# Optimization experiments

Hardware: AMD Instinct MI355X
Metric: run time of the kernel (lower is better)

## Reference

```python
import jax, jax.numpy as jnp
import numpy as np

B_, T_, D_ = 4, 4096, 512
H_, DH_ = 8, 64
N_HASHES, BUCKET = 4, 64
SELF_ATTN_VAL = -5e4  # TOKEN_SELF_ATTN_VALUE from reformer-pytorch


def setup_inputs() -> dict:
    key = jax.random.key(0)
    ks = jax.random.split(key, 12)
    s = 0.02
    return {
        "src": jax.random.normal(ks[0], (B_, T_, D_), jnp.float32),
        "Wqk": jax.random.normal(ks[1], (D_, D_), jnp.float32) * s,
        "Wv": jax.random.normal(ks[2], (D_, D_), jnp.float32) * s,
        "Wout": jax.random.normal(ks[3], (D_, D_), jnp.float32) * s,
        "bout": jnp.zeros((D_,), jnp.float32),
        "W1": jax.random.normal(ks[4], (D_, 2048), jnp.float32) * s,
        "b1": jnp.zeros((2048,), jnp.float32),
        "W2": jax.random.normal(ks[5], (2048, D_), jnp.float32) * s,
        "b2": jnp.zeros((D_,), jnp.float32),
        "gamma": jnp.ones((D_,), jnp.float32),
        "beta": jnp.zeros((D_,), jnp.float32),
        "rotations": jax.random.normal(ks[6], (DH_, N_HASHES, (T_ // BUCKET) // 2), jnp.float32),
    }


def _look_one_back(x):
    # concat each chunk with the previous chunk (wraparound), along the slot axis
    prev = jnp.concatenate([x[:, -1:], x[:, :-1]], axis=1)
    return jnp.concatenate([x, prev], axis=2)


def lsh_attention(qk, v, rotations):
    # qk, v: (B, T, d) with B = batch*heads; shared-QK LSH attention (non-causal,
    # attend_across_buckets=True, allow_duplicate_attention=True, no dropout)
    B, T, d = qk.shape
    n_buckets = T // BUCKET
    # --- hashing ---
    rv = jnp.einsum("btf,fhi->bhti", qk, rotations)          # (B, n_hashes, T, nb/2)
    rv = jnp.concatenate([rv, -rv], axis=-1)                  # (B, n_hashes, T, nb)
    buckets = jnp.argmax(rv, axis=-1)                         # (B, n_hashes, T)
    offsets = (jnp.arange(N_HASHES) * n_buckets)[None, :, None]
    buckets = (buckets + offsets).reshape(B, N_HASHES * T)
    # --- sort by (bucket, position) ---
    ticker = jnp.arange(N_HASHES * T)
    buckets_and_t = buckets * T + (ticker % T)[None, :]
    sticker = jnp.argsort(buckets_and_t, axis=-1)             # (B, n_hashes*T)
    undo_sort = jnp.argsort(sticker, axis=-1)
    st = sticker % T
    sqk = jnp.take_along_axis(qk, st[..., None], axis=1)      # (B, n_hashes*T, d)
    sv = jnp.take_along_axis(v, st[..., None], axis=1)
    # --- chunk ---
    chunks = N_HASHES * n_buckets
    bq_t = st.reshape(B, chunks, BUCKET)
    bqk = sqk.reshape(B, chunks, BUCKET, d)
    bv = sv.reshape(B, chunks, BUCKET, d)
    bq = bqk
    bk = bqk / (jnp.linalg.norm(bqk, axis=-1, keepdims=True) + 1e-6)
    bk = _look_one_back(bk)                                   # (B, chunks, 2*BUCKET, d)
    bv = _look_one_back(bv)
    bkv_t = _look_one_back(bq_t)                              # (B, chunks, 2*BUCKET)
    # --- attention within chunk (+ one look-back chunk) ---
    dots = jnp.einsum("bcie,bcje->bcij", bq, bk) * (d ** -0.5)
    self_mask = bq_t[:, :, :, None] == bkv_t[:, :, None, :]
    dots = jnp.where(self_mask, SELF_ATTN_VAL, dots)
    lse = jax.nn.logsumexp(dots, axis=-1, keepdims=True)
    p = jnp.exp(dots - lse)
    bo = jnp.einsum("bcij,bcje->bcie", p, bv)
    # --- unsort and combine hash rounds ---
    so = bo.reshape(B, N_HASHES * T, d)
    slog = lse.reshape(B, N_HASHES * T)
    o = jnp.take_along_axis(so, undo_sort[..., None], axis=1)
    logits = jnp.take_along_axis(slog, undo_sort, axis=1)
    o = o.reshape(B, N_HASHES, T, d)
    logits = logits.reshape(B, N_HASHES, T, 1)
    probs = jnp.exp(logits - jax.nn.logsumexp(logits, axis=1, keepdims=True))
    return jnp.sum(o * probs, axis=1)                         # (B, T, d)


def _layer(src, Wqk, Wv, Wout, bout, W1, b1, W2, b2, gamma, beta, rotations):
    b, t, dm = src.shape
    qk = src @ Wqk
    v = src @ Wv
    def split(x):
        return x.reshape(b, t, H_, DH_).transpose(0, 2, 1, 3).reshape(b * H_, t, DH_)
    o = lsh_attention(split(qk), split(v), rotations)
    o = o.reshape(b, H_, t, DH_).transpose(0, 2, 1, 3).reshape(b, t, dm)
    attn_out = o @ Wout + bout
    x = src + attn_out                # residual (dropout = identity in eval)
    ffn = jax.nn.relu(x @ W1 + b1) @ W2 + b2
    y = x + ffn
    mu = jnp.mean(y, axis=-1, keepdims=True)
    var = jnp.mean((y - mu) ** 2, axis=-1, keepdims=True)
    return (y - mu) / jnp.sqrt(var + 1e-6) * gamma + beta     # post-norm (norm2)


def reference(src, Wqk, Wv, Wout, bout, W1, b1, W2, b2, gamma, beta, rotations):
    return _layer(src, Wqk, Wv, Wout, bout, W1, b1, W2, b2, gamma, beta, rotations)
```

## Files before the change

kernel.cpp:

```cpp
#include <hip/hip_runtime.h>

#define B_ 4
#define T_ 4096
#define D_ 512
#define H_ 8
#define DH_ 64
#define NH_ 4
#define NB_ 64
#define BH_ (B_*H_)
#define CHUNKS_ (NH_*NB_)
#define NTICK_ (NH_*T_)
#define M_ (B_*T_)
#define FFN_ 2048

typedef __attribute__((ext_vector_type(8))) short bf16x8;
typedef __attribute__((ext_vector_type(4))) float f32x4;

__device__ __forceinline__ unsigned short f2bf(float x) {
  unsigned int u = __float_as_uint(x);
  return (unsigned short)((u + 0x7FFFu + ((u >> 16) & 1u)) >> 16);
}
__device__ __forceinline__ float bf2f(unsigned short s) {
  return __uint_as_float(((unsigned int)s) << 16);
}
__device__ __forceinline__ unsigned int cvt_pk_bf16(float lo, float hi) {
  unsigned int r;
  asm("v_cvt_pk_bf16_f32 %0, %1, %2" : "=v"(r) : "v"(lo), "v"(hi));
  return r;
}

__device__ __forceinline__ void gld_lds16(const void* g, void* l) {
  __builtin_amdgcn_global_load_lds(
      (const __attribute__((address_space(1))) unsigned int*)g,
      (__attribute__((address_space(3))) unsigned int*)l, 16, 0, 0);
}

__device__ __forceinline__ int off64(int row, int k) {
  return row * 64 + (((k >> 3) ^ ((row ^ (row >> 3)) & 7)) << 3) + (k & 7);
}
__device__ __forceinline__ int off128(int row, int k) {
  return row * 128 + (((k >> 3) ^ ((row ^ (row >> 3)) & 7)) << 3) + (k & 7);
}

template<int BM, int OUT_MODE, bool HAS_BIAS, bool RELU, bool HAS_RESID, bool FUSE_INV>
__global__ __launch_bounds__(256) void gemm_bf16(
    const unsigned short* __restrict__ A, const unsigned short* __restrict__ BT,
    const float* __restrict__ bias, const unsigned short* __restrict__ resid,
    float* __restrict__ Cf, unsigned short* __restrict__ Cb,
    float* __restrict__ invn,
    int M, int N, int K, int lda, int ldbt, int ldr)
{
  constexpr int MI = BM / 32;
  __shared__ __align__(16) unsigned short smem[(BM + 128) * 64];
  unsigned short* As = smem;
  unsigned short* Bs = smem + BM * 64;
  const int tid = threadIdx.x;
  const int lane = tid & 63;
  const int w = tid >> 6;
  const int wm = (w >> 1) * (BM / 2), wn = (w & 1) * 64;
  const int g = lane >> 4, cl = lane & 15;

  const int gx = gridDim.x;
  const int id = blockIdx.x + blockIdx.y * gx;
  const int cpx = (gx * gridDim.y) >> 3;
  const int swz = (id & 7) * cpx + (id >> 3);
  const int m0 = (swz / gx) * BM, n0 = (swz % gx) * 128;

  f32x4 acc[MI][4];
#pragma unroll
  for (int i = 0; i < MI; ++i)
#pragma unroll
    for (int j = 0; j < 4; ++j) acc[i][j] = (f32x4){0.f, 0.f, 0.f, 0.f};

  const int srow = tid >> 3;
  const int skc  = (tid & 7) * 8;

  for (int k0 = 0; k0 < K; k0 += 64) {
#pragma unroll
    for (int ci = 0; ci < BM / 32; ++ci)
      gld_lds16(&A[(size_t)(m0 + ci * 32 + srow) * lda + k0 + skc],
                &As[ci * 2048 + tid * 8]);
#pragma unroll
    for (int ci = 0; ci < 4; ++ci)
      gld_lds16(&BT[(size_t)(n0 + ci * 32 + srow) * ldbt + k0 + skc],
                &Bs[ci * 2048 + tid * 8]);
    __syncthreads();
#pragma unroll
    for (int kk = 0; kk < 64; kk += 32) {
      bf16x8 af[MI], bfr[4];
#pragma unroll
      for (int i = 0; i < MI; ++i)
        af[i] = *(const bf16x8*)&As[(wm + i * 16 + cl) * 64 + kk + g * 8];
#pragma unroll
      for (int j = 0; j < 4; ++j)
        bfr[j] = *(const bf16x8*)&Bs[(wn + j * 16 + cl) * 64 + kk + g * 8];
#pragma unroll
      for (int i = 0; i < MI; ++i)
#pragma unroll
        for (int j = 0; j < 4; ++j)
          acc[i][j] = __builtin_amdgcn_mfma_f32_16x16x32_bf16(af[i], bfr[j], acc[i][j], 0, 0, 0);
    }
    __syncthreads();
  }

  float bv[4];
  if constexpr (HAS_BIAS) {
#pragma unroll
    for (int j = 0; j < 4; ++j) bv[j] = bias[n0 + wn + j * 16 + cl];
  }
#pragma unroll
  for (int i = 0; i < MI; ++i) {
#pragma unroll
    for (int r = 0; r < 4; ++r) {
      const int lrow = wm + i * 16 + g * 4 + r;
      float v4[4];
      float ss = 0.f;
#pragma unroll
      for (int j = 0; j < 4; ++j) {
        float val = acc[i][j][r];
        if constexpr (HAS_BIAS) val += bv[j];
        if constexpr (RELU) val = fmaxf(val, 0.f);
        v4[j] = val;
        if constexpr (FUSE_INV) ss += val * val;
        if constexpr (OUT_MODE == 2)
          Cf[(size_t)(m0 + lrow) * N + n0 + wn + j * 16 + cl] = val;
      }
      const unsigned int p01 = cvt_pk_bf16(v4[0], v4[1]);
      const unsigned int p23 = cvt_pk_bf16(v4[2], v4[3]);
      const int sw = (lrow & 7) << 3;
      smem[lrow * 128 + ((wn +  0 + cl) ^ sw)] = (unsigned short)p01;
      smem[lrow * 128 + ((wn + 16 + cl) ^ sw)] = (unsigned short)(p01 >> 16);
      smem[lrow * 128 + ((wn + 32 + cl) ^ sw)] = (unsigned short)p23;
      smem[lrow * 128 + ((wn + 48 + cl) ^ sw)] = (unsigned short)(p23 >> 16);
      if constexpr (FUSE_INV) {
        ss += __shfl_xor(ss, 1); ss += __shfl_xor(ss, 2);
        ss += __shfl_xor(ss, 4); ss += __shfl_xor(ss, 8);
        if (cl == 0) {
          const int m = m0 + lrow;
          const int bb = m >> 12, t = m & (T_ - 1);
          const int hh = ((n0 + wn) >> 6) & 7;
          invn[((size_t)(bb * 8 + hh)) * T_ + t] = 1.0f / (sqrtf(ss) + 1e-6f);
        }
      }
    }
  }
  __syncthreads();
#pragma unroll
  for (int l = 0; l < BM / 16; ++l) {
    const int idx = tid + l * 256;
    const int row = idx >> 4, c8 = (idx & 15) * 8;
    uint4 u = *(const uint4*)&smem[row * 128 + (c8 ^ ((row & 7) << 3))];
    if constexpr (HAS_RESID) {
      const uint4 rv = *(const uint4*)&resid[(size_t)(m0 + row) * ldr + n0 + c8];
      const unsigned short* sp = (const unsigned short*)&u;
      const unsigned short* rp = (const unsigned short*)&rv;
      float f[8];
#pragma unroll
      for (int e = 0; e < 8; ++e) f[e] = bf2f(sp[e]) + bf2f(rp[e]);
      u.x = cvt_pk_bf16(f[0], f[1]); u.y = cvt_pk_bf16(f[2], f[3]);
      u.z = cvt_pk_bf16(f[4], f[5]); u.w = cvt_pk_bf16(f[6], f[7]);
    }
    *(uint4*)&Cb[(size_t)(m0 + row) * N + n0 + c8] = u;
  }
}

__global__ __launch_bounds__(256) void prep_all(
    const float* __restrict__ Wqk, const float* __restrict__ Wv,
    const float* __restrict__ Wout, const float* __restrict__ W1,
    const float* __restrict__ W2, const float* __restrict__ src,
    unsigned short* __restrict__ WqkTp, unsigned short* __restrict__ WvT,
    unsigned short* __restrict__ WoutT, unsigned short* __restrict__ W1T,
    unsigned short* __restrict__ W2T, unsigned short* __restrict__ src_pair)
{
  __shared__ float tile[32][33];
  int bid = blockIdx.x;
  if (bid >= 2816) {
    const int i = (bid - 2816) * 256 + threadIdx.x;
    const int gpr = D_ >> 3;
    const int m = i / gpr, d0 = (i - m * gpr) * 8;
    float x[8];
    *(float4*)&x[0] = *(const float4*)&src[(size_t)m * D_ + d0];
    *(float4*)&x[4] = *(const float4*)&src[(size_t)m * D_ + d0 + 4];
    unsigned short hi[8], lo[8];
#pragma unroll
    for (int e = 0; e < 8; ++e) {
      hi[e] = f2bf(x[e]);
      lo[e] = f2bf(x[e] - bf2f(hi[e]));
    }
    *(uint4*)&src_pair[(size_t)m * 2 * D_ + d0]      = *(const uint4*)&hi[0];
    *(uint4*)&src_pair[(size_t)m * 2 * D_ + D_ + d0] = *(const uint4*)&lo[0];
    return;
  }
  const float* W; unsigned short* WT; int K, N, bx, by; bool split = false;
  if (bid < 256)        { W = Wqk;  WT = WqkTp; K = 512;  N = 512;  split = true;
                          bx = bid & 15; by = bid >> 4; }
  else if (bid < 512)   { bid -= 256;  W = Wv;   WT = WvT;   K = 512;  N = 512;
                          bx = bid & 15; by = bid >> 4; }
  else if (bid < 768)   { bid -= 512;  W = Wout; WT = WoutT; K = 512;  N = 512;
                          bx = bid & 15; by = bid >> 4; }
  else if (bid < 1792)  { bid -= 768;  W = W1;   WT = W1T;   K = 512;  N = 2048;
                          bx = bid & 63; by = bid >> 6; }
  else                  { bid -= 1792; W = W2;   WT = W2T;   K = 2048; N = 512;
                          bx = bid & 15; by = bid >> 4; }
  const int k0 = by * 32, n0 = bx * 32;
  const int tx = threadIdx.x & 31, ty = threadIdx.x >> 5;
#pragma unroll
  for (int r = 0; r < 32; r += 8)
    tile[ty + r][tx] = W[(size_t)(k0 + ty + r) * N + n0 + tx];
  __syncthreads();
  const int ld = split ? 2 * K : K;
#pragma unroll
  for (int r = 0; r < 32; r += 8) {
    const float x = tile[tx][ty + r];
    const unsigned short hi = f2bf(x);
    WT[(size_t)(n0 + ty + r) * ld + k0 + tx] = hi;
    if (split)
      WT[(size_t)(n0 + ty + r) * ld + K + k0 + tx] = f2bf(x - bf2f(hi));
  }
}

__global__ __launch_bounds__(256) void hash_gemm_kernel(
    const float* __restrict__ qk, const float* __restrict__ rot,
    int* __restrict__ buckets)
{
  __shared__ __align__(16) float As[64][136];
  __shared__ __align__(16) float Bs[64][132];
  const int tid = threadIdx.x;
  const int tx = tid & 15, ty = tid >> 4;
  const int t0 = blockIdx.x * 128, bh = blockIdx.y;
  const int b = bh >> 3, hd = bh & 7;

#pragma unroll
  for (int l = 0; l < 8; ++l) {
    const int idx = tid + l * 256;
    const int row = idx >> 4;
    const int kq = (idx & 15) << 2;
    const float4 a = *(const float4*)&qk[((size_t)b * T_ + t0 + row) * D_ + hd * DH_ + kq];
    As[kq + 0][row] = a.x; As[kq + 1][row] = a.y;
    As[kq + 2][row] = a.z; As[kq + 3][row] = a.w;
  }
#pragma unroll
  for (int l = 0; l < 8; ++l) {
    const int idx = tid + l * 256;
    const int kr = idx >> 5;
    const int c4 = (idx & 31) << 2;
    *(float4*)&Bs[kr][c4] = *(const float4*)&rot[kr * 128 + c4];
  }
  __syncthreads();

  float acc[8][8];
#pragma unroll
  for (int i = 0; i < 8; ++i)
#pragma unroll
    for (int j = 0; j < 8; ++j) acc[i][j] = 0.f;

#pragma unroll 4
  for (int kk = 0; kk < 64; ++kk) {
    float a[8], bq[8];
    *(float4*)&a[0]  = *(const float4*)&As[kk][ty * 8];
    *(float4*)&a[4]  = *(const float4*)&As[kk][ty * 8 + 4];
    *(float4*)&bq[0] = *(const float4*)&Bs[kk][tx * 8];
    *(float4*)&bq[4] = *(const float4*)&Bs[kk][tx * 8 + 4];
#pragma unroll
    for (int i = 0; i < 8; ++i)
#pragma unroll
      for (int j = 0; j < 8; ++j)
        acc[i][j] = fmaf(a[i], bq[j], acc[i][j]);
  }
  __syncthreads();

  float* pval = &As[0][0];
  int*   pidx = (int*)&Bs[0][0];
  const int i0 = (tx & 3) * 8;
#pragma unroll
  for (int r = 0; r < 8; ++r) {
    float v = -3.0e38f; int idx = 127;
#pragma unroll
    for (int j = 0; j < 8; ++j) {
      const float p = acc[r][j];
      const int li = i0 + j;
      if (p > v || (p == v && li < idx)) { v = p; idx = li; }
      const float n = -p;
      const int ni = 32 + li;
      if (n > v || (n == v && ni < idx)) { v = n; idx = ni; }
    }
    pval[(ty * 8 + r) * 16 + tx] = v;
    pidx[(ty * 8 + r) * 16 + tx] = idx;
  }
  __syncthreads();

#pragma unroll
  for (int l = 0; l < 2; ++l) {
    const int id = tid + l * 256;
    const int tok = id >> 2, hh = id & 3;
    float v = pval[tok * 16 + hh * 4];
    int idx = pidx[tok * 16 + hh * 4];
#pragma unroll
    for (int e = 1; e < 4; ++e) {
      const float ov = pval[tok * 16 + hh * 4 + e];
      const int oi = pidx[tok * 16 + hh * 4 + e];
      if (ov > v || (ov == v && oi < idx)) { v = ov; idx = oi; }
    }
    buckets[((size_t)bh * NH_ + hh) * T_ + t0 + tok] = idx + hh * NB_;
  }
}

__global__ __launch_bounds__(256) void hist_kernel(
    const int* __restrict__ buckets, int* __restrict__ bstart)
{
  __shared__ int bins[256];
  const int bh = blockIdx.x;
  bins[threadIdx.x] = 0;
  __syncthreads();
  for (int e = threadIdx.x; e < NTICK_; e += 256)
    atomicAdd(&bins[buckets[(size_t)bh * NTICK_ + e]], 1);
  __syncthreads();
  if (threadIdx.x == 0) {
    int run = 0;
    for (int i = 0; i < 256; ++i) { const int c = bins[i]; bins[i] = run; run += c; }
  }
  __syncthreads();
  bstart[bh * 256 + threadIdx.x] = bins[threadIdx.x];
}

__global__ __launch_bounds__(64) void compact_kernel(
    const int* __restrict__ buckets, const int* __restrict__ bstart,
    int* __restrict__ sticker)
{
  const int bucket = blockIdx.x, bh = blockIdx.y;
  const int h = bucket >> 6;
  const int lane = threadIdx.x;
  int base = bstart[bh * 256 + bucket];
  const int* bk = buckets + (size_t)bh * NTICK_ + (size_t)h * T_;
  for (int it = 0; it < 64; ++it) {
    const int t = it * 64 + lane;
    const bool m = (bk[t] == bucket);
    const unsigned long long bal = __ballot(m);
    if (m) {
      const int pos = base + __popcll(bal & ((1ull << lane) - 1ull));
      sticker[(size_t)bh * NTICK_ + pos] = h * T_ + t;
    }
    base += __popcll(bal);
  }
}

__global__ __launch_bounds__(256) void attn_kernel(
    const unsigned short* __restrict__ qkb, const unsigned short* __restrict__ vb,
    const int* __restrict__ sticker, const float* __restrict__ invn,
    unsigned short* __restrict__ orowsb, float* __restrict__ logits)
{
  __shared__ __align__(16) unsigned short Rs[128 * 64];
  __shared__ __align__(16) unsigned short Vs[128 * 64];
  __shared__ int tks[128];
  __shared__ float invs[128];

  const int cx = blockIdx.x;
  const int c = (cx & 7) * 32 + (cx >> 3);
  const int bh = blockIdx.y;
  const int b = bh >> 3, hd = bh & 7;
  const int tid = threadIdx.x;
  const int hr = c >> 6;
  const int w = tid >> 6, lane = tid & 63, g = lane >> 4, cl = lane & 15;

  if (tid < 128) {
    const int sc = (tid < 64) ? c : ((c + CHUNKS_ - 1) & (CHUNKS_ - 1));
    const int tick = sticker[(size_t)bh * NTICK_ + sc * 64 + (tid & 63)];
    const int t = tick & (T_ - 1);
    tks[tid] = t;
    invs[tid] = invn[bh * T_ + t];
  }
  __syncthreads();

#pragma unroll
  for (int l = 0; l < 4; ++l) {
    const int idx = tid + l * 256;
    const int row = idx >> 3, k0 = (idx & 7) * 8;
    const size_t gb = ((size_t)b * T_ + tks[row]) * D_ + hd * DH_ + k0;
    *(uint4*)&Rs[off64(row, k0)] = *(const uint4*)&qkb[gb];
    *(uint4*)&Vs[off64(row, k0)] = *(const uint4*)&vb[gb];
  }
  __syncthreads();

  f32x4 sacc[8];
#pragma unroll
  for (int j = 0; j < 8; ++j) sacc[j] = (f32x4){0.f, 0.f, 0.f, 0.f};
  __builtin_amdgcn_s_setprio(1);
#pragma unroll
  for (int kk = 0; kk < 2; ++kk) {
    const bf16x8 aq = *(const bf16x8*)&Rs[off64(w * 16 + cl, kk * 32 + g * 8)];
#pragma unroll
    for (int j = 0; j < 8; ++j) {
      const bf16x8 bk = *(const bf16x8*)&Rs[off64(j * 16 + cl, kk * 32 + g * 8)];
      sacc[j] = __builtin_amdgcn_mfma_f32_16x16x32_bf16(aq, bk, sacc[j], 0, 0, 0);
    }
  }
  __builtin_amdgcn_s_setprio(0);
  const int d0 = (tid & 15) * 4, tg = tid >> 4;
  unsigned int qw[8][2];
#pragma unroll
  for (int e = 0; e < 8; ++e) {
    const uint2 q = *(const uint2*)&Vs[off64(tg * 8 + e, d0)];
    qw[e][0] = q.x; qw[e][1] = q.y;
  }
  __syncthreads();

  {
    unsigned short col[4][8];
#pragma unroll
    for (int e = 0; e < 8; ++e) {
      col[0][e] = (unsigned short)(qw[e][0] & 0xffffu);
      col[1][e] = (unsigned short)(qw[e][0] >> 16);
      col[2][e] = (unsigned short)(qw[e][1] & 0xffffu);
      col[3][e] = (unsigned short)(qw[e][1] >> 16);
    }
#pragma unroll
    for (int dd = 0; dd < 4; ++dd)
      *(uint4*)&Vs[off128(d0 + dd, tg * 8)] = *(const uint4*)&col[dd][0];
  }

  float iv[8]; int tk[8];
#pragma unroll
  for (int j = 0; j < 8; ++j) {
    iv[j] = invs[j * 16 + cl] * 0.125f;
    tk[j] = tks[j * 16 + cl];
  }
  float pinv[4];
#pragma unroll
  for (int r = 0; r < 4; ++r) {
    const int row = w * 16 + g * 4 + r;
    const int tq = tks[row];
    float e8[8];
    float sum = 0.f;
#pragma unroll
    for (int j = 0; j < 8; ++j) {
      float e = __expf(sacc[j][r] * iv[j]);
      if (tq == tk[j]) e = 0.f;
      e8[j] = e;
      sum += e;
    }
    sum += __shfl_xor(sum, 1); sum += __shfl_xor(sum, 2);
    sum += __shfl_xor(sum, 4); sum += __shfl_xor(sum, 8);
    pinv[r] = 1.f / sum;
#pragma unroll
    for (int j = 0; j < 8; j += 2) {
      const unsigned int pk = cvt_pk_bf16(e8[j], e8[j + 1]);
      Rs[off128(row, j * 16 + cl)]       = (unsigned short)pk;
      Rs[off128(row, (j + 1) * 16 + cl)] = (unsigned short)(pk >> 16);
    }
    if (cl == 0)
      logits[((size_t)bh * T_ + tq) * NH_ + hr] = __logf(sum);
  }
  __syncthreads();

  f32x4 oacc[4];
#pragma unroll
  for (int jd = 0; jd < 4; ++jd) oacc[jd] = (f32x4){0.f, 0.f, 0.f, 0.f};
  __builtin_amdgcn_s_setprio(1);
#pragma unroll
  for (int ks = 0; ks < 4; ++ks) {
    const bf16x8 pa = *(const bf16x8*)&Rs[off128(w * 16 + cl, ks * 32 + g * 8)];
#pragma unroll
    for (int jd = 0; jd < 4; ++jd) {
      const bf16x8 vv = *(const bf16x8*)&Vs[off128(jd * 16 + cl, ks * 32 + g * 8)];
      oacc[jd] = __builtin_amdgcn_mfma_f32_16x16x32_bf16(pa, vv, oacc[jd], 0, 0, 0);
    }
  }
  __builtin_amdgcn_s_setprio(0);
  __syncthreads();

#pragma unroll
  for (int r = 0; r < 4; ++r) {
    const int row = w * 16 + g * 4 + r;
    const unsigned int q01 = cvt_pk_bf16(oacc[0][r] * pinv[r], oacc[1][r] * pinv[r]);
    const unsigned int q23 = cvt_pk_bf16(oacc[2][r] * pinv[r], oacc[3][r] * pinv[r]);
    Rs[off64(row,      cl)] = (unsigned short)q01;
    Rs[off64(row, 16 + cl)] = (unsigned short)(q01 >> 16);
    Rs[off64(row, 32 + cl)] = (unsigned short)q23;
    Rs[off64(row, 48 + cl)] = (unsigned short)(q23 >> 16);
  }
  __syncthreads();

#pragma unroll
  for (int l = 0; l < 2; ++l) {
    const int idx = tid + l * 256;
    const int row = idx >> 3, k0 = (idx & 7) * 8;
    *(uint4*)&orowsb[(((size_t)bh * T_ + tks[row]) * NH_ + hr) * DH_ + k0] =
        *(const uint4*)&Rs[off64(row, k0)];
  }
}

__global__ __launch_bounds__(256) void combine_kernel(
    const unsigned short* __restrict__ orowsb, const float* __restrict__ logits,
    unsigned short* __restrict__ ocombb)
{
  const int gid = blockIdx.x * 4 + (threadIdx.x >> 6);
  const int lane = threadIdx.x & 63;
  const int bh = gid >> 12, t = gid & (T_ - 1);
  const int b = bh >> 3, hd = bh & 7;
  const float4 lg = *(const float4*)&logits[((size_t)bh * T_ + t) * NH_];
  const float m = fmaxf(fmaxf(lg.x, lg.y), fmaxf(lg.z, lg.w));
  const float w0 = __expf(lg.x - m), w1 = __expf(lg.y - m);
  const float w2 = __expf(lg.z - m), w3 = __expf(lg.w - m);
  const float inv = 1.f / (w0 + w1 + w2 + w3);
  const size_t rb = ((size_t)bh * T_ + t) * (NH_ * DH_) + lane;
  const float o = w0 * bf2f(orowsb[rb])
                + w1 * bf2f(orowsb[rb + DH_])
                + w2 * bf2f(orowsb[rb + 2 * DH_])
                + w3 * bf2f(orowsb[rb + 3 * DH_]);
  ocombb[((size_t)b * T_ + t) * D_ + hd * DH_ + lane] = f2bf(o * inv);
}

__global__ __launch_bounds__(256) void ln_kernel(
    const unsigned short* __restrict__ yb, const float* __restrict__ gamma,
    const float* __restrict__ beta, float* __restrict__ out)
{
  const int row = blockIdx.x * 4 + (threadIdx.x >> 6);
  const int lane = threadIdx.x & 63;
  const size_t base = (size_t)row * D_ + lane * 8;
  const uint4 u = *(const uint4*)&yb[base];
  const unsigned short* up = (const unsigned short*)&u;
  float x[8];
#pragma unroll
  for (int i = 0; i < 8; ++i) x[i] = bf2f(up[i]);
  float s = 0.f;
#pragma unroll
  for (int i = 0; i < 8; ++i) s += x[i];
#pragma unroll
  for (int m = 32; m >= 1; m >>= 1) s += __shfl_xor(s, m);
  const float mu = s * (1.f / D_);
  float vs = 0.f;
#pragma unroll
  for (int i = 0; i < 8; ++i) { const float d = x[i] - mu; vs += d * d; }
#pragma unroll
  for (int m = 32; m >= 1; m >>= 1) vs += __shfl_xor(vs, m);
  const float rstd = rsqrtf(vs * (1.f / D_) + 1e-6f);
  float gm[8], bt[8];
  *(float4*)&gm[0] = *(const float4*)&gamma[lane * 8];
  *(float4*)&gm[4] = *(const float4*)&gamma[lane * 8 + 4];
  *(float4*)&bt[0] = *(const float4*)&beta[lane * 8];
  *(float4*)&bt[4] = *(const float4*)&beta[lane * 8 + 4];
  float o[8];
#pragma unroll
  for (int i = 0; i < 8; ++i) o[i] = (x[i] - mu) * rstd * gm[i] + bt[i];
  *(float4*)&out[base]     = make_float4(o[0], o[1], o[2], o[3]);
  *(float4*)&out[base + 4] = make_float4(o[4], o[5], o[6], o[7]);
}

extern "C" void kernel_launch(void* const* d_in, const int* in_sizes, int n_in,
                              void* d_out, int out_size, void* d_ws, size_t ws_size,
                              hipStream_t stream) {
  (void)in_sizes; (void)n_in; (void)out_size; (void)ws_size;
  const float* src   = (const float*)d_in[0];
  const float* Wqk   = (const float*)d_in[1];
  const float* Wv    = (const float*)d_in[2];
  const float* Wout  = (const float*)d_in[3];
  const float* bout  = (const float*)d_in[4];
  const float* W1    = (const float*)d_in[5];
  const float* b1    = (const float*)d_in[6];
  const float* W2    = (const float*)d_in[7];
  const float* b2    = (const float*)d_in[8];
  const float* gamma = (const float*)d_in[9];
  const float* beta  = (const float*)d_in[10];
  const float* rot   = (const float*)d_in[11];
  float* out = (float*)d_out;

  char* ws = (char*)d_ws;
  const size_t MB = 1024 * 1024;
  float*          qk       = (float*)(ws);
  unsigned short* src_pair = (unsigned short*)(ws + 32 * MB);
  unsigned short* v_b      = (unsigned short*)(ws + 64 * MB);
  unsigned short* orows_b  = (unsigned short*)(ws + 80 * MB);
  unsigned short* qk_b     = (unsigned short*)(ws + 144 * MB);
  char* p = ws + 160 * MB;
  float* logits  = (float*)p; p += (size_t)BH_ * NH_ * T_ * 4;
  int*   buckets = (int*)p;   p += (size_t)BH_ * NH_ * T_ * 4;
  int*   sticker = (int*)p;   p += (size_t)BH_ * NTICK_ * 4;
  int*   bstart  = (int*)p;   p += (size_t)BH_ * 256 * 4;
  float* invn    = (float*)p; p += (size_t)BH_ * T_ * 4;
  unsigned short* WvT    = (unsigned short*)p; p += (size_t)D_ * D_ * 2;
  unsigned short* WoutT  = (unsigned short*)p; p += (size_t)D_ * D_ * 2;
  unsigned short* W1T    = (unsigned short*)p; p += (size_t)FFN_ * D_ * 2;
  unsigned short* W2T    = (unsigned short*)p; p += (size_t)D_ * FFN_ * 2;
  unsigned short* WqkTp  = (unsigned short*)p; p += (size_t)D_ * 2 * D_ * 2;

  unsigned short* ocomb_b  = qk_b;
  unsigned short* x_b      = v_b;
  unsigned short* hidden_b = orows_b;
  unsigned short* ybuf_b   = (unsigned short*)ws;

  prep_all<<<2816 + M_ * D_ / 8 / 256, 256, 0, stream>>>(
      Wqk, Wv, Wout, W1, W2, src, WqkTp, WvT, WoutT, W1T, W2T, src_pair);

  gemm_bf16<64, 2, false, false, false, true><<<dim3(D_ / 128, M_ / 64), 256, 0, stream>>>(
      src_pair, WqkTp, nullptr, nullptr, qk, qk_b, invn, M_, D_, 2 * D_, 2 * D_, 2 * D_, 0);
  gemm_bf16<64, 1, false, false, false, false><<<dim3(D_ / 128, M_ / 64), 256, 0, stream>>>(
      src_pair, WvT, nullptr, nullptr, nullptr, v_b, nullptr, M_, D_, D_, 2 * D_, D_, 0);
  hash_gemm_kernel<<<dim3(T_ / 128, BH_), 256, 0, stream>>>(qk, rot, buckets);
  hist_kernel<<<BH_, 256, 0, stream>>>(buckets, bstart);
  compact_kernel<<<dim3(256, BH_), 64, 0, stream>>>(buckets, bstart, sticker);
  attn_kernel<<<dim3(CHUNKS_, BH_), 256, 0, stream>>>(
      qk_b, v_b, sticker, invn, orows_b, logits);
  combine_kernel<<<BH_ * T_ / 4, 256, 0, stream>>>(orows_b, logits, ocomb_b);
  gemm_bf16<64, 1, true, false, true, false><<<dim3(D_ / 128, M_ / 64), 256, 0, stream>>>(
      ocomb_b, WoutT, bout, src_pair, nullptr, x_b, nullptr, M_, D_, D_, D_, D_, 2 * D_);
  gemm_bf16<128, 1, true, true, false, false><<<dim3(FFN_ / 128, M_ / 128), 256, 0, stream>>>(
      x_b, W1T, b1, nullptr, nullptr, hidden_b, nullptr, M_, FFN_, D_, D_, D_, 0);
  gemm_bf16<64, 1, true, false, true, false><<<dim3(D_ / 128, M_ / 64), 256, 0, stream>>>(
      hidden_b, W2T, b2, x_b, nullptr, ybuf_b, nullptr, M_, D_, FFN_, FFN_, FFN_, D_);
  ln_kernel<<<M_ / 4, 256, 0, stream>>>(ybuf_b, gamma, beta, out);
}
```

Before: 369.8 us.

## Fuse QK and V projections, drop split-bf16 precision, use async LDS gathers

```diff
diff --git a/kernel.cpp b/kernel.cpp
--- a/kernel.cpp
+++ b/kernel.cpp
@@ -35,19 +35,20 @@
       (__attribute__((address_space(3))) unsigned int*)l, 16, 0, 0);
 }
 
+__device__ __forceinline__ int swf(int row) { return (row ^ (row >> 3)) & 7; }
 __device__ __forceinline__ int off64(int row, int k) {
-  return row * 64 + (((k >> 3) ^ ((row ^ (row >> 3)) & 7)) << 3) + (k & 7);
+  return row * 64 + (((k >> 3) ^ swf(row)) << 3) + (k & 7);
 }
 __device__ __forceinline__ int off128(int row, int k) {
-  return row * 128 + (((k >> 3) ^ ((row ^ (row >> 3)) & 7)) << 3) + (k & 7);
-}
-
-template<int BM, int OUT_MODE, bool HAS_BIAS, bool RELU, bool HAS_RESID, bool FUSE_INV>
+  return row * 128 + (((k >> 3) ^ swf(row)) << 3) + (k & 7);
+}
+
+template<int BM, int MODE, bool HAS_BIAS, bool RELU, bool HAS_RESID>
 __global__ __launch_bounds__(256) void gemm_bf16(
     const unsigned short* __restrict__ A, const unsigned short* __restrict__ BT,
     const float* __restrict__ bias, const unsigned short* __restrict__ resid,
     float* __restrict__ Cf, unsigned short* __restrict__ Cb,
-    float* __restrict__ invn,
+    unsigned short* __restrict__ Cb2, float* __restrict__ invn,
     int M, int N, int K, int lda, int ldbt, int ldr)
 {
   constexpr int MI = BM / 32;
@@ -66,6 +67,8 @@
   const int swz = (id & 7) * cpx + (id >> 3);
   const int m0 = (swz / gx) * BM, n0 = (swz % gx) * 128;
 
+  const bool isv = (MODE == 3) && (n0 >= 512);
+
   f32x4 acc[MI][4];
 #pragma unroll
   for (int i = 0; i < MI; ++i)
@@ -121,9 +124,12 @@
         if constexpr (HAS_BIAS) val += bv[j];
         if constexpr (RELU) val = fmaxf(val, 0.f);
         v4[j] = val;
-        if constexpr (FUSE_INV) ss += val * val;
-        if constexpr (OUT_MODE == 2)
-          Cf[(size_t)(m0 + lrow) * N + n0 + wn + j * 16 + cl] = val;
+        if constexpr (MODE == 3) {
+          if (!isv) {
+            ss += val * val;
+            Cf[(size_t)(m0 + lrow) * 512 + n0 + wn + j * 16 + cl] = val;
+          }
+        }
       }
       const unsigned int p01 = cvt_pk_bf16(v4[0], v4[1]);
       const unsigned int p23 = cvt_pk_bf16(v4[2], v4[3]);
@@ -132,14 +138,16 @@
       smem[lrow * 128 + ((wn + 16 + cl) ^ sw)] = (unsigned short)(p01 >> 16);
       smem[lrow * 128 + ((wn + 32 + cl) ^ sw)] = (unsigned short)p23;
       smem[lrow * 128 + ((wn + 48 + cl) ^ sw)] = (unsigned short)(p23 >> 16);
-      if constexpr (FUSE_INV) {
-        ss += __shfl_xor(ss, 1); ss += __shfl_xor(ss, 2);
-        ss += __shfl_xor(ss, 4); ss += __shfl_xor(ss, 8);
-        if (cl == 0) {
-          const int m = m0 + lrow;
-          const int bb = m >> 12, t = m & (T_ - 1);
-          const int hh = ((n0 + wn) >> 6) & 7;
-          invn[((size_t)(bb * 8 + hh)) * T_ + t] = 1.0f / (sqrtf(ss) + 1e-6f);
+      if constexpr (MODE == 3) {
+        if (!isv) {
+          ss += __shfl_xor(ss, 1); ss += __shfl_xor(ss, 2);
+          ss += __shfl_xor(ss, 4); ss += __shfl_xor(ss, 8);
+          if (cl == 0) {
+            const int m = m0 + lrow;
+            const int bb = m >> 12, t = m & (T_ - 1);
+            const int hh = ((n0 + wn) >> 6) & 7;
+            invn[((size_t)(bb * 8 + hh)) * T_ + t] = 1.0f / (sqrtf(ss) + 1e-6f);
+          }
         }
       }
     }
@@ -160,7 +168,14 @@
       u.x = cvt_pk_bf16(f[0], f[1]); u.y = cvt_pk_bf16(f[2], f[3]);
       u.z = cvt_pk_bf16(f[4], f[5]); u.w = cvt_pk_bf16(f[6], f[7]);
     }
-    *(uint4*)&Cb[(size_t)(m0 + row) * N + n0 + c8] = u;
+    if constexpr (MODE == 3) {
+      if (isv)
+        *(uint4*)&Cb2[(size_t)(m0 + row) * 512 + (n0 - 512) + c8] = u;
+      else
+        *(uint4*)&Cb[(size_t)(m0 + row) * 512 + n0 + c8] = u;
+    } else {
+      *(uint4*)&Cb[(size_t)(m0 + row) * N + n0 + c8] = u;
+    }
   }
 }
 
@@ -168,33 +183,29 @@
     const float* __restrict__ Wqk, const float* __restrict__ Wv,
     const float* __restrict__ Wout, const float* __restrict__ W1,
     const float* __restrict__ W2, const float* __restrict__ src,
-    unsigned short* __restrict__ WqkTp, unsigned short* __restrict__ WvT,
-    unsigned short* __restrict__ WoutT, unsigned short* __restrict__ W1T,
-    unsigned short* __restrict__ W2T, unsigned short* __restrict__ src_pair)
+    unsigned short* __restrict__ WqkvT, unsigned short* __restrict__ WoutT,
+    unsigned short* __restrict__ W1T, unsigned short* __restrict__ W2T,
+    unsigned short* __restrict__ src_b)
 {
   __shared__ float tile[32][33];
   int bid = blockIdx.x;
   if (bid >= 2816) {
     const int i = (bid - 2816) * 256 + threadIdx.x;
-    const int gpr = D_ >> 3;
-    const int m = i / gpr, d0 = (i - m * gpr) * 8;
+    const int m = i >> 6, d0 = (i & 63) * 8;
     float x[8];
     *(float4*)&x[0] = *(const float4*)&src[(size_t)m * D_ + d0];
     *(float4*)&x[4] = *(const float4*)&src[(size_t)m * D_ + d0 + 4];
-    unsigned short hi[8], lo[8];
-#pragma unroll
-    for (int e = 0; e < 8; ++e) {
-      hi[e] = f2bf(x[e]);
-      lo[e] = f2bf(x[e] - bf2f(hi[e]));
-    }
-    *(uint4*)&src_pair[(size_t)m * 2 * D_ + d0]      = *(const uint4*)&hi[0];
-    *(uint4*)&src_pair[(size_t)m * 2 * D_ + D_ + d0] = *(const uint4*)&lo[0];
+    unsigned short hi[8];
+#pragma unroll
+    for (int e = 0; e < 8; ++e) hi[e] = f2bf(x[e]);
+    *(uint4*)&src_b[(size_t)m * D_ + d0] = *(const uint4*)&hi[0];
     return;
   }
-  const float* W; unsigned short* WT; int K, N, bx, by; bool split = false;
-  if (bid < 256)        { W = Wqk;  WT = WqkTp; K = 512;  N = 512;  split = true;
+  const float* W; unsigned short* WT; int K, N, bx, by;
+  if (bid < 256)        { W = Wqk;  WT = WqkvT; K = 512;  N = 512;
                           bx = bid & 15; by = bid >> 4; }
-  else if (bid < 512)   { bid -= 256;  W = Wv;   WT = WvT;   K = 512;  N = 512;
+  else if (bid < 512)   { bid -= 256;  W = Wv; WT = WqkvT + (size_t)512 * 512;
+                          K = 512; N = 512;
                           bx = bid & 15; by = bid >> 4; }
   else if (bid < 768)   { bid -= 512;  W = Wout; WT = WoutT; K = 512;  N = 512;
                           bx = bid & 15; by = bid >> 4; }
@@ -208,15 +219,9 @@
   for (int r = 0; r < 32; r += 8)
     tile[ty + r][tx] = W[(size_t)(k0 + ty + r) * N + n0 + tx];
   __syncthreads();
-  const int ld = split ? 2 * K : K;
-#pragma unroll
-  for (int r = 0; r < 32; r += 8) {
-    const float x = tile[tx][ty + r];
-    const unsigned short hi = f2bf(x);
-    WT[(size_t)(n0 + ty + r) * ld + k0 + tx] = hi;
-    if (split)
-      WT[(size_t)(n0 + ty + r) * ld + K + k0 + tx] = f2bf(x - bf2f(hi));
-  }
+#pragma unroll
+  for (int r = 0; r < 32; r += 8)
+    WT[(size_t)(n0 + ty + r) * K + k0 + tx] = f2bf(tile[tx][ty + r]);
 }
 
 __global__ __launch_bounds__(256) void hash_gemm_kernel(
@@ -371,13 +376,17 @@
   }
   __syncthreads();
 
-#pragma unroll
-  for (int l = 0; l < 4; ++l) {
-    const int idx = tid + l * 256;
-    const int row = idx >> 3, k0 = (idx & 7) * 8;
-    const size_t gb = ((size_t)b * T_ + tks[row]) * D_ + hd * DH_ + k0;
-    *(uint4*)&Rs[off64(row, k0)] = *(const uint4*)&qkb[gb];
-    *(uint4*)&Vs[off64(row, k0)] = *(const uint4*)&vb[gb];
+  {
+    const int sr = lane >> 3, gq = lane & 7;
+#pragma unroll
+    for (int l = 0; l < 4; ++l) {
+      const int row = l * 32 + w * 8 + sr;
+      const size_t gb = ((size_t)b * T_ + tks[row]) * D_ + hd * DH_
+                      + ((gq ^ swf(row)) << 3);
+      const int dst = (l * 32 + w * 8) * 64 + lane * 8;
+      gld_lds16(&qkb[gb], &Rs[dst]);
+      gld_lds16(&vb[gb],  &Vs[dst]);
+    }
   }
   __syncthreads();
 
@@ -566,22 +575,21 @@
 
   char* ws = (char*)d_ws;
   const size_t MB = 1024 * 1024;
-  float*          qk       = (float*)(ws);
-  unsigned short* src_pair = (unsigned short*)(ws + 32 * MB);
-  unsigned short* v_b      = (unsigned short*)(ws + 64 * MB);
-  unsigned short* orows_b  = (unsigned short*)(ws + 80 * MB);
-  unsigned short* qk_b     = (unsigned short*)(ws + 144 * MB);
-  char* p = ws + 160 * MB;
-  float* logits  = (float*)p; p += (size_t)BH_ * NH_ * T_ * 4;
+  float*          qk      = (float*)(ws);
+  unsigned short* src_b   = (unsigned short*)(ws + 32 * MB);
+  unsigned short* v_b     = (unsigned short*)(ws + 48 * MB);
+  unsigned short* orows_b = (unsigned short*)(ws + 64 * MB);
+  unsigned short* qk_b    = (unsigned short*)(ws + 128 * MB);
+  char* p = ws + 144 * MB;
+  float* logits  = (float*)p; p += (size_t)BH_ * T_ * NH_ * 4;
   int*   buckets = (int*)p;   p += (size_t)BH_ * NH_ * T_ * 4;
   int*   sticker = (int*)p;   p += (size_t)BH_ * NTICK_ * 4;
   int*   bstart  = (int*)p;   p += (size_t)BH_ * 256 * 4;
   float* invn    = (float*)p; p += (size_t)BH_ * T_ * 4;
-  unsigned short* WvT    = (unsigned short*)p; p += (size_t)D_ * D_ * 2;
-  unsigned short* WoutT  = (unsigned short*)p; p += (size_t)D_ * D_ * 2;
-  unsigned short* W1T    = (unsigned short*)p; p += (size_t)FFN_ * D_ * 2;
-  unsigned short* W2T    = (unsigned short*)p; p += (size_t)D_ * FFN_ * 2;
-  unsigned short* WqkTp  = (unsigned short*)p; p += (size_t)D_ * 2 * D_ * 2;
+  unsigned short* WqkvT = (unsigned short*)p; p += (size_t)1024 * 512 * 2;
+  unsigned short* WoutT = (unsigned short*)p; p += (size_t)D_ * D_ * 2;
+  unsigned short* W1T   = (unsigned short*)p; p += (size_t)FFN_ * D_ * 2;
+  unsigned short* W2T   = (unsigned short*)p; p += (size_t)D_ * FFN_ * 2;
 
   unsigned short* ocomb_b  = qk_b;
   unsigned short* x_b      = v_b;
@@ -589,23 +597,29 @@
   unsigned short* ybuf_b   = (unsigned short*)ws;
 
   prep_all<<<2816 + M_ * D_ / 8 / 256, 256, 0, stream>>>(
-      Wqk, Wv, Wout, W1, W2, src, WqkTp, WvT, WoutT, W1T, W2T, src_pair);
-
-  gemm_bf16<64, 2, false, false, false, true><<<dim3(D_ / 128, M_ / 64), 256, 0, stream>>>(
-      src_pair, WqkTp, nullptr, nullptr, qk, qk_b, invn, M_, D_, 2 * D_, 2 * D_, 2 * D_, 0);
-  gemm_bf16<64, 1, false, false, false, false><<<dim3(D_ / 128, M_ / 64), 256, 0, stream>>>(
-      src_pair, WvT, nullptr, nullptr, nullptr, v_b, nullptr, M_, D_, D_, 2 * D_, D_, 0);
+      Wqk, Wv, Wout, W1, W2, src, WqkvT, WoutT, W1T, W2T, src_b);
+
+  gemm_bf16<128, 3, false, false, false>
+      <<<dim3(1024 / 128, M_ / 128), 256, 0, stream>>>(
+      src_b, WqkvT, nullptr, nullptr, qk, qk_b, v_b, invn,
+      M_, 1024, D_, D_, D_, 0);
   hash_gemm_kernel<<<dim3(T_ / 128, BH_), 256, 0, stream>>>(qk, rot, buckets);
   hist_kernel<<<BH_, 256, 0, stream>>>(buckets, bstart);
   compact_kernel<<<dim3(256, BH_), 64, 0, stream>>>(buckets, bstart, sticker);
   attn_kernel<<<dim3(CHUNKS_, BH_), 256, 0, stream>>>(
       qk_b, v_b, sticker, invn, orows_b, logits);
   combine_kernel<<<BH_ * T_ / 4, 256, 0, stream>>>(orows_b, logits, ocomb_b);
-  gemm_bf16<64, 1, true, false, true, false><<<dim3(D_ / 128, M_ / 64), 256, 0, stream>>>(
-      ocomb_b, WoutT, bout, src_pair, nullptr, x_b, nullptr, M_, D_, D_, D_, D_, 2 * D_);
-  gemm_bf16<128, 1, true, true, false, false><<<dim3(FFN_ / 128, M_ / 128), 256, 0, stream>>>(
-      x_b, W1T, b1, nullptr, nullptr, hidden_b, nullptr, M_, FFN_, D_, D_, D_, 0);
-  gemm_bf16<64, 1, true, false, true, false><<<dim3(D_ / 128, M_ / 64), 256, 0, stream>>>(
-      hidden_b, W2T, b2, x_b, nullptr, ybuf_b, nullptr, M_, D_, FFN_, FFN_, FFN_, D_);
+  gemm_bf16<128, 1, true, false, true>
+      <<<dim3(D_ / 128, M_ / 128), 256, 0, stream>>>(
+      ocomb_b, WoutT, bout, src_b, nullptr, x_b, nullptr, nullptr,
+      M_, D_, D_, D_, D_, D_);
+  gemm_bf16<128, 1, true, true, false>
+      <<<dim3(FFN_ / 128, M_ / 128), 256, 0, stream>>>(
+      x_b, W1T, b1, nullptr, nullptr, hidden_b, nullptr, nullptr,
+      M_, FFN_, D_, D_, D_, 0);
+  gemm_bf16<128, 1, true, false, true>
+      <<<dim3(D_ / 128, M_ / 128), 256, 0, stream>>>(
+      hidden_b, W2T, b2, x_b, nullptr, ybuf_b, nullptr, nullptr,
+      M_, D_, FFN_, FFN_, FFN_, D_);
   ln_kernel<<<M_ / 4, 256, 0, stream>>>(ybuf_b, gamma, beta, out);
 }
```

Result: faster. 353.0 us (-4.5%).
